# Optimization experiments

Hardware: AMD Instinct MI355X
Metric: run time of the kernel (lower is better)

## Reference

```python
import jax, jax.numpy as jnp
import numpy as np

SX = 4.0
SY = 4.0
H_DIM = 1024
B = 128
FH, FW = 24, 48


def setup_inputs() -> dict:
    key = jax.random.key(0)
    ks = jax.random.split(key, 8)
    s = lambda fan_in: 1.0 / np.sqrt(fan_in)
    return {
        "inp": jax.random.normal(ks[0], (B, H_DIM), jnp.float32),
        "hid": jax.random.normal(ks[1], (B, H_DIM), jnp.float32),
        "V": jax.random.normal(ks[2], (FH, FW, B, H_DIM), jnp.float32),
        "W1": jax.random.normal(ks[3], (2 * H_DIM, H_DIM), jnp.float32) * s(H_DIM),
        "b1": jnp.zeros((2 * H_DIM,), jnp.float32),
        "W2": jax.random.normal(ks[4], (2, 2 * H_DIM), jnp.float32) * s(2 * H_DIM),
        "b2": jnp.zeros((2,), jnp.float32),
        "Wc": jax.random.normal(ks[5], (H_DIM, 2 * H_DIM), jnp.float32) * s(2 * H_DIM),
        "bc": jnp.zeros((H_DIM,), jnp.float32),
    }


def reference(inp, hid, V, W1, b1, W2, b2, Wc, bc):
    h, w = V.shape[0], V.shape[1]
    # alignment MLP: Linear -> tanh -> Linear -> sigmoid, output [B, 2]
    algn = jax.nn.sigmoid(jnp.tanh(hid @ W1.T + b1) @ W2.T + b2)
    px, py = algn[:, 0], algn[:, 1]           # [B]
    x0 = (px * w)[:, None, None]              # [B,1,1]
    y0 = (py * h)[:, None, None]
    xs = jnp.arange(w, dtype=V.dtype)[None, None, :]   # [1,1,w]
    ys = jnp.arange(h, dtype=V.dtype)[None, :, None]   # [1,h,1]
    # Gaussian window weights over the feature map, [B,h,w]
    alpha = jnp.exp(-((xs - x0) ** 2 / (2.0 * SX * SX)
                      + (ys - y0) ** 2 / (2.0 * SY * SY)))
    alpha = alpha / alpha.sum(axis=(1, 2), keepdims=True)
    # weighted pooling over spatial dims: [B,h,w] x [h,w,B,H] -> [B,H]
    attn = jnp.einsum('brc,rcbh->bh', alpha, V)
    # contextualizer: Linear(2H, H) + ReLU on concat([inp, attn])
    ctx = jax.nn.relu(jnp.concatenate([inp, attn], axis=1) @ Wc.T + bc)
    return ctx
```

## Files before the change

### kernel.cpp

```cpp
#include <hip/hip_runtime.h>
#include <math.h>

#define NB 128
#define HD 1024
#define FHH 24
#define FWW 48

#define OFF_TPART 0u
#define OFF_X0    2097152u
#define OFF_Y0    2097280u
#define OFF_WXN   2097408u
#define OFF_WYN   2103552u
#define OFF_ATTN  2106624u

__global__ __launch_bounds__(256) void k_gemm1(
    const float* __restrict__ hid, const float* __restrict__ W1,
    float* __restrict__ tpart) {
  __shared__ float xs[32][132];
  __shared__ float wsh[32][36];
  const int tid = threadIdx.x;
  const int jt = blockIdx.x;
  const int ks = blockIdx.y;
  const int ty = tid >> 3, tx = tid & 7;
  const int b0 = ty * 4, jl = tx * 4;
  float acc[4][4] = {{0.f, 0.f, 0.f, 0.f}};
  for (int kt = 0; kt < 4; ++kt) {
    const int k0 = ks * 128 + kt * 32;
#pragma unroll
    for (int i = 0; i < 4; ++i) {
      int idx = tid + 256 * i;
      int bb = idx >> 3, q = idx & 7;
      float4 g = *(const float4*)(hid + bb * 1024 + k0 + q * 4);
      xs[q * 4 + 0][bb] = g.x;
      xs[q * 4 + 1][bb] = g.y;
      xs[q * 4 + 2][bb] = g.z;
      xs[q * 4 + 3][bb] = g.w;
    }
    {
      int o = tid >> 3, q = tid & 7;
      float4 g = *(const float4*)(W1 + (size_t)(jt * 32 + o) * 1024 + k0 + q * 4);
      wsh[q * 4 + 0][o] = g.x;
      wsh[q * 4 + 1][o] = g.y;
      wsh[q * 4 + 2][o] = g.z;
      wsh[q * 4 + 3][o] = g.w;
    }
    __syncthreads();
#pragma unroll
    for (int kk = 0; kk < 32; ++kk) {
      float4 xa = *(const float4*)&xs[kk][b0];
      float4 wb = *(const float4*)&wsh[kk][jl];
      acc[0][0] = fmaf(xa.x, wb.x, acc[0][0]);
      acc[0][1] = fmaf(xa.x, wb.y, acc[0][1]);
      acc[0][2] = fmaf(xa.x, wb.z, acc[0][2]);
      acc[0][3] = fmaf(xa.x, wb.w, acc[0][3]);
      acc[1][0] = fmaf(xa.y, wb.x, acc[1][0]);
      acc[1][1] = fmaf(xa.y, wb.y, acc[1][1]);
      acc[1][2] = fmaf(xa.y, wb.z, acc[1][2]);
      acc[1][3] = fmaf(xa.y, wb.w, acc[1][3]);
      acc[2][0] = fmaf(xa.z, wb.x, acc[2][0]);
      acc[2][1] = fmaf(xa.z, wb.y, acc[2][1]);
      acc[2][2] = fmaf(xa.z, wb.z, acc[2][2]);
      acc[2][3] = fmaf(xa.z, wb.w, acc[2][3]);
      acc[3][0] = fmaf(xa.w, wb.x, acc[3][0]);
      acc[3][1] = fmaf(xa.w, wb.y, acc[3][1]);
      acc[3][2] = fmaf(xa.w, wb.z, acc[3][2]);
      acc[3][3] = fmaf(xa.w, wb.w, acc[3][3]);
    }
    __syncthreads();
  }
#pragma unroll
  for (int u = 0; u < 4; ++u) {
    float4 o;
    o.x = acc[u][0]; o.y = acc[u][1]; o.z = acc[u][2]; o.w = acc[u][3];
    *(float4*)(tpart + (size_t)ks * 262144u + (size_t)(b0 + u) * 2048u +
               (jt * 32 + jl)) = o;
  }
}

__global__ __launch_bounds__(256) void k_align(
    const float* __restrict__ tpart, const float* __restrict__ b1,
    const float* __restrict__ W2, const float* __restrict__ b2,
    float* __restrict__ x0a, float* __restrict__ y0a,
    float* __restrict__ wxn, float* __restrict__ wyn) {
  const int b = blockIdx.x;
  const int tid = threadIdx.x;
  float a0 = 0.f, a1 = 0.f;
#pragma unroll
  for (int i = 0; i < 8; ++i) {
    int j = tid + 256 * i;
    float s = b1[j];
#pragma unroll
    for (int ks = 0; ks < 8; ++ks)
      s += tpart[(size_t)ks * 262144u + (size_t)b * 2048u + j];
    float tv = tanhf(s);
    a0 += tv * W2[j];
    a1 += tv * W2[2048 + j];
  }
  __shared__ float r0[256], r1[256];
  r0[tid] = a0; r1[tid] = a1;
  __syncthreads();
  for (int s = 128; s > 0; s >>= 1) {
    if (tid < s) { r0[tid] += r0[tid + s]; r1[tid] += r1[tid + s]; }
    __syncthreads();
  }
  __shared__ float xy[2];
  __shared__ float wxl[48], wyl[24];
  __shared__ float invZ[2];
  if (tid == 0) {
    float p0 = 1.f / (1.f + expf(-(r0[0] + b2[0])));
    float p1 = 1.f / (1.f + expf(-(r1[0] + b2[1])));
    xy[0] = p0 * 48.f;
    xy[1] = p1 * 24.f;
  }
  __syncthreads();
  float x0 = xy[0], y0 = xy[1];
  if (tid < 48) {
    float d = (float)tid - x0;
    wxl[tid] = expf(-d * d * (1.f / 32.f));
  } else if (tid >= 64 && tid < 88) {
    int r = tid - 64;
    float d = (float)r - y0;
    wyl[r] = expf(-d * d * (1.f / 32.f));
  }
  __syncthreads();
  if (tid == 0) {
    float zx = 0.f, zy = 0.f;
    for (int c = 0; c < 48; ++c) zx += wxl[c];
    for (int r = 0; r < 24; ++r) zy += wyl[r];
    invZ[0] = 1.f / zx;
    invZ[1] = 1.f / zy;
  }
  __syncthreads();
  if (tid < 48) wxn[b * 48 + tid] = wxl[tid] * invZ[0];
  else if (tid >= 64 && tid < 88) wyn[b * 24 + (tid - 64)] = wyl[tid - 64] * invZ[1];
  if (tid == 0) { x0a[b] = x0; y0a[b] = y0; }
}

__global__ __launch_bounds__(512) void k_attn(
    const float* __restrict__ V, const float* __restrict__ x0a,
    const float* __restrict__ y0a, const float* __restrict__ wxn,
    const float* __restrict__ wyn, float* __restrict__ attn) {
  const int b = blockIdx.x;
  const int qtr = blockIdx.y;
  const int tid = threadIdx.x;
  const int w = tid >> 6;
  const int lane = tid & 63;
  __shared__ float wxl[48], wyl[24];
  __shared__ float xy[2];
  __shared__ float red[8][260];
  if (tid < 48) wxl[tid] = wxn[b * 48 + tid];
  else if (tid >= 64 && tid < 88) wyl[tid - 64] = wyn[b * 24 + (tid - 64)];
  if (tid == 96) xy[0] = x0a[b];
  if (tid == 97) xy[1] = y0a[b];
  __syncthreads();
  const float x0 = xy[0], y0 = xy[1];
  const int h0 = qtr * 256 + lane * 4;
  float4 acc; acc.x = 0.f; acc.y = 0.f; acc.z = 0.f; acc.w = 0.f;
  const int rlo = max(0, (int)ceilf(y0 - 12.f));
  const int rhi = min(23, (int)floorf(y0 + 12.f));
  for (int r = w; r < 24; r += 8) {
    if (r < rlo || r > rhi) continue;
    float dy = (float)r - y0;
    float rad = sqrtf(fmaxf(144.f - dy * dy, 0.f));
    int c0 = max(0, (int)ceilf(x0 - rad));
    int c1 = min(47, (int)floorf(x0 + rad));
    float wy = wyl[r];
    const float* base = V + ((size_t)((r * 48 + c0) * 128 + b)) * 1024u + h0;
#pragma unroll 4
    for (int c = c0; c <= c1; ++c) {
      float wgt = wy * wxl[c];
      const float4 v = *(const float4*)(base + (size_t)(c - c0) * 131072u);
      acc.x = fmaf(wgt, v.x, acc.x);
      acc.y = fmaf(wgt, v.y, acc.y);
      acc.z = fmaf(wgt, v.z, acc.z);
      acc.w = fmaf(wgt, v.w, acc.w);
    }
  }
  *(float4*)&red[w][lane * 4] = acc;
  __syncthreads();
  if (tid < 256) {
    float s = 0.f;
#pragma unroll
    for (int ww = 0; ww < 8; ++ww) s += red[ww][tid];
    attn[(size_t)b * 1024u + qtr * 256 + tid] = s;
  }
}

__global__ __launch_bounds__(256) void k_gemm2(
    const float* __restrict__ inp, const float* __restrict__ attn,
    const float* __restrict__ Wc, float* __restrict__ psum) {
  __shared__ float xs[32][132];
  __shared__ float wsh[32][36];
  const int tid = threadIdx.x;
  const int ot = blockIdx.x;
  const int ks = blockIdx.y;
  const int ty = tid >> 3, tx = tid & 7;
  const int b0 = ty * 4, ol = tx * 4;
  const float* xsrc = (ks < 4) ? inp : attn;
  const int kbase = (ks < 4) ? ks * 256 : (ks - 4) * 256;
  float acc[4][4] = {{0.f, 0.f, 0.f, 0.f}};
  for (int kt = 0; kt < 8; ++kt) {
    const int k0g = ks * 256 + kt * 32;
    const int k0x = kbase + kt * 32;
#pragma unroll
    for (int i = 0; i < 4; ++i) {
      int idx = tid + 256 * i;
      int bb = idx >> 3, q = idx & 7;
      float4 g = *(const float4*)(xsrc + bb * 1024 + k0x + q * 4);
      xs[q * 4 + 0][bb] = g.x;
      xs[q * 4 + 1][bb] = g.y;
      xs[q * 4 + 2][bb] = g.z;
      xs[q * 4 + 3][bb] = g.w;
    }
    {
      int o = tid >> 3, q = tid & 7;
      float4 g = *(const float4*)(Wc + (size_t)(ot * 32 + o) * 2048u + k0g + q * 4);
      wsh[q * 4 + 0][o] = g.x;
      wsh[q * 4 + 1][o] = g.y;
      wsh[q * 4 + 2][o] = g.z;
      wsh[q * 4 + 3][o] = g.w;
    }
    __syncthreads();
#pragma unroll
    for (int kk = 0; kk < 32; ++kk) {
      float4 xa = *(const float4*)&xs[kk][b0];
      float4 wb = *(const float4*)&wsh[kk][ol];
      acc[0][0] = fmaf(xa.x, wb.x, acc[0][0]);
      acc[0][1] = fmaf(xa.x, wb.y, acc[0][1]);
      acc[0][2] = fmaf(xa.x, wb.z, acc[0][2]);
      acc[0][3] = fmaf(xa.x, wb.w, acc[0][3]);
      acc[1][0] = fmaf(xa.y, wb.x, acc[1][0]);
      acc[1][1] = fmaf(xa.y, wb.y, acc[1][1]);
      acc[1][2] = fmaf(xa.y, wb.z, acc[1][2]);
      acc[1][3] = fmaf(xa.y, wb.w, acc[1][3]);
      acc[2][0] = fmaf(xa.z, wb.x, acc[2][0]);
      acc[2][1] = fmaf(xa.z, wb.y, acc[2][1]);
      acc[2][2] = fmaf(xa.z, wb.z, acc[2][2]);
      acc[2][3] = fmaf(xa.z, wb.w, acc[2][3]);
      acc[3][0] = fmaf(xa.w, wb.x, acc[3][0]);
      acc[3][1] = fmaf(xa.w, wb.y, acc[3][1]);
      acc[3][2] = fmaf(xa.w, wb.z, acc[3][2]);
      acc[3][3] = fmaf(xa.w, wb.w, acc[3][3]);
    }
    __syncthreads();
  }
#pragma unroll
  for (int u = 0; u < 4; ++u) {
    float4 o;
    o.x = acc[u][0]; o.y = acc[u][1]; o.z = acc[u][2]; o.w = acc[u][3];
    *(float4*)(psum + (size_t)ks * 131072u + (size_t)(b0 + u) * 1024u +
               (ot * 32 + ol)) = o;
  }
}

__global__ __launch_bounds__(256) void k_final(
    const float* __restrict__ psum, const float* __restrict__ bc,
    float* __restrict__ out) {
  const int gid = blockIdx.x * 256 + threadIdx.x;
  const int o = gid & 1023;
  float s = bc[o];
#pragma unroll
  for (int i = 0; i < 8; ++i) s += psum[(size_t)i * 131072u + gid];
  out[gid] = fmaxf(s, 0.f);
}

extern "C" void kernel_launch(void* const* d_in, const int* in_sizes, int n_in,
                              void* d_out, int out_size, void* d_ws,
                              size_t ws_size, hipStream_t stream) {
  const float* inp = (const float*)d_in[0];
  const float* hid = (const float*)d_in[1];
  const float* V   = (const float*)d_in[2];
  const float* W1  = (const float*)d_in[3];
  const float* b1  = (const float*)d_in[4];
  const float* W2  = (const float*)d_in[5];
  const float* b2  = (const float*)d_in[6];
  const float* Wc  = (const float*)d_in[7];
  const float* bc  = (const float*)d_in[8];
  float* out = (float*)d_out;
  float* ws = (float*)d_ws;

  float* tpart = ws + OFF_TPART;
  float* x0a   = ws + OFF_X0;
  float* y0a   = ws + OFF_Y0;
  float* wxn   = ws + OFF_WXN;
  float* wyn   = ws + OFF_WYN;
  float* attn  = ws + OFF_ATTN;

  k_gemm1<<<dim3(64, 8), 256, 0, stream>>>(hid, W1, tpart);
  k_align<<<128, 256, 0, stream>>>(tpart, b1, W2, b2, x0a, y0a, wxn, wyn);
  k_attn<<<dim3(128, 4), 512, 0, stream>>>(V, x0a, y0a, wxn, wyn, attn);
  k_gemm2<<<dim3(32, 8), 256, 0, stream>>>(inp, attn, Wc, tpart);
  k_final<<<512, 256, 0, stream>>>(tpart, bc, out);
}
```

Baseline: 743.1 us.

## Flatten Gaussian window cells into balanced per-batch list for attention gather

k_align now computes the truncated window's cells once per batch: flat V offsets plus combined normalized weights, padded to a multiple of 64. k_attn stages this list in shared memory, and each warp walks an even, strided share of it with 8-way unrolled vector loads. This replaces the per-row split, where each warp took whole rows of uneven length and redid the bounds maths. Loads of V are marked nontemporal. The cost is extra workspace writes and reads for the cell list and a small amount of padded zero-weight work.

```diff
diff --git a/kernel.cpp b/kernel.cpp
--- a/kernel.cpp
+++ b/kernel.cpp
@@ -5,13 +5,15 @@
 #define HD 1024
 #define FHH 24
 #define FWW 48
+#define MAXCELL 640
+
+typedef float f4 __attribute__((ext_vector_type(4)));
 
 #define OFF_TPART 0u
-#define OFF_X0    2097152u
-#define OFF_Y0    2097280u
-#define OFF_WXN   2097408u
-#define OFF_WYN   2103552u
-#define OFF_ATTN  2106624u
+#define OFF_NC    2097152u
+#define OFF_COFF  2097280u
+#define OFF_CWTS  2179200u
+#define OFF_ATTN  2261120u
 
 __global__ __launch_bounds__(256) void k_gemm1(
     const float* __restrict__ hid, const float* __restrict__ W1,
@@ -80,8 +82,8 @@
 __global__ __launch_bounds__(256) void k_align(
     const float* __restrict__ tpart, const float* __restrict__ b1,
     const float* __restrict__ W2, const float* __restrict__ b2,
-    float* __restrict__ x0a, float* __restrict__ y0a,
-    float* __restrict__ wxn, float* __restrict__ wyn) {
+    int* __restrict__ ncnt, unsigned* __restrict__ goffs,
+    float* __restrict__ gwts) {
   const int b = blockIdx.x;
   const int tid = threadIdx.x;
   float a0 = 0.f, a1 = 0.f;
@@ -113,7 +115,7 @@
     xy[1] = p1 * 24.f;
   }
   __syncthreads();
-  float x0 = xy[0], y0 = xy[1];
+  const float x0 = xy[0], y0 = xy[1];
   if (tid < 48) {
     float d = (float)tid - x0;
     wxl[tid] = expf(-d * d * (1.f / 32.f));
@@ -131,52 +133,80 @@
     invZ[1] = 1.f / zy;
   }
   __syncthreads();
-  if (tid < 48) wxn[b * 48 + tid] = wxl[tid] * invZ[0];
-  else if (tid >= 64 && tid < 88) wyn[b * 24 + (tid - 64)] = wyl[tid - 64] * invZ[1];
-  if (tid == 0) { x0a[b] = x0; y0a[b] = y0; }
+  __shared__ int c0s[24], cnts[24], rowst[24];
+  __shared__ int tot[2];
+  const int rlo = max(0, (int)ceilf(y0 - 12.f));
+  const int rhi = min(23, (int)floorf(y0 + 12.f));
+  if (tid < 24) {
+    int cnt = 0, c0 = 0;
+    if (tid >= rlo && tid <= rhi) {
+      float dy = (float)tid - y0;
+      float rad = sqrtf(fmaxf(144.f - dy * dy, 0.f));
+      c0 = max(0, (int)ceilf(x0 - rad));
+      int c1 = min(47, (int)floorf(x0 + rad));
+      cnt = (c1 >= c0) ? (c1 - c0 + 1) : 0;
+    }
+    c0s[tid] = c0;
+    cnts[tid] = cnt;
+  }
+  __syncthreads();
+  if (tid == 0) {
+    int run = 0;
+    for (int r = 0; r < 24; ++r) { rowst[r] = run; run += cnts[r]; }
+    tot[0] = run;
+    tot[1] = (run + 63) & ~63;
+  }
+  __syncthreads();
+  const float izx = invZ[0], izy = invZ[1];
+#pragma unroll
+  for (int r = 0; r < 24; ++r) {
+    if (tid < cnts[r]) {
+      int c = c0s[r] + tid;
+      int e = rowst[r] + tid;
+      goffs[b * MAXCELL + e] = (unsigned)((r * 48 + c) * 128 + b) * 1024u;
+      gwts[b * MAXCELL + e] = (wyl[r] * izy) * (wxl[c] * izx);
+    }
+  }
+  for (int e = tot[0] + tid; e < tot[1]; e += 256) {
+    goffs[b * MAXCELL + e] = 0u;
+    gwts[b * MAXCELL + e] = 0.f;
+  }
+  if (tid == 0) ncnt[b] = tot[1];
 }
 
 __global__ __launch_bounds__(512) void k_attn(
-    const float* __restrict__ V, const float* __restrict__ x0a,
-    const float* __restrict__ y0a, const float* __restrict__ wxn,
-    const float* __restrict__ wyn, float* __restrict__ attn) {
+    const float* __restrict__ V, const int* __restrict__ ncnt,
+    const unsigned* __restrict__ goffs, const float* __restrict__ gwts,
+    float* __restrict__ attn) {
   const int b = blockIdx.x;
   const int qtr = blockIdx.y;
   const int tid = threadIdx.x;
   const int w = tid >> 6;
   const int lane = tid & 63;
-  __shared__ float wxl[48], wyl[24];
-  __shared__ float xy[2];
-  __shared__ float red[8][260];
-  if (tid < 48) wxl[tid] = wxn[b * 48 + tid];
-  else if (tid >= 64 && tid < 88) wyl[tid - 64] = wyn[b * 24 + (tid - 64)];
-  if (tid == 96) xy[0] = x0a[b];
-  if (tid == 97) xy[1] = y0a[b];
-  __syncthreads();
-  const float x0 = xy[0], y0 = xy[1];
+  __shared__ unsigned offs_l[MAXCELL];
+  __shared__ float wts_l[MAXCELL];
+  const int npad = ncnt[b];
+  for (int i = tid; i < npad; i += 512) {
+    offs_l[i] = goffs[b * MAXCELL + i];
+    wts_l[i] = gwts[b * MAXCELL + i];
+  }
+  __syncthreads();
   const int h0 = qtr * 256 + lane * 4;
-  float4 acc; acc.x = 0.f; acc.y = 0.f; acc.z = 0.f; acc.w = 0.f;
-  const int rlo = max(0, (int)ceilf(y0 - 12.f));
-  const int rhi = min(23, (int)floorf(y0 + 12.f));
-  for (int r = w; r < 24; r += 8) {
-    if (r < rlo || r > rhi) continue;
-    float dy = (float)r - y0;
-    float rad = sqrtf(fmaxf(144.f - dy * dy, 0.f));
-    int c0 = max(0, (int)ceilf(x0 - rad));
-    int c1 = min(47, (int)floorf(x0 + rad));
-    float wy = wyl[r];
-    const float* base = V + ((size_t)((r * 48 + c0) * 128 + b)) * 1024u + h0;
-#pragma unroll 4
-    for (int c = c0; c <= c1; ++c) {
-      float wgt = wy * wxl[c];
-      const float4 v = *(const float4*)(base + (size_t)(c - c0) * 131072u);
+  f4 acc = {0.f, 0.f, 0.f, 0.f};
+  for (int t = w * 8; t < npad; t += 64) {
+#pragma unroll
+    for (int u = 0; u < 8; ++u) {
+      unsigned off = offs_l[t + u];
+      float wgt = wts_l[t + u];
+      f4 v = __builtin_nontemporal_load((const f4*)(V + off + h0));
       acc.x = fmaf(wgt, v.x, acc.x);
       acc.y = fmaf(wgt, v.y, acc.y);
       acc.z = fmaf(wgt, v.z, acc.z);
       acc.w = fmaf(wgt, v.w, acc.w);
     }
   }
-  *(float4*)&red[w][lane * 4] = acc;
+  __shared__ float red[8][260];
+  *(f4*)&red[w][lane * 4] = acc;
   __syncthreads();
   if (tid < 256) {
     float s = 0.f;
@@ -279,16 +309,15 @@
   float* out = (float*)d_out;
   float* ws = (float*)d_ws;
 
-  float* tpart = ws + OFF_TPART;
-  float* x0a   = ws + OFF_X0;
-  float* y0a   = ws + OFF_Y0;
-  float* wxn   = ws + OFF_WXN;
-  float* wyn   = ws + OFF_WYN;
-  float* attn  = ws + OFF_ATTN;
+  float* tpart    = ws + OFF_TPART;
+  int* ncnt       = (int*)(ws + OFF_NC);
+  unsigned* goffs = (unsigned*)(ws + OFF_COFF);
+  float* gwts     = ws + OFF_CWTS;
+  float* attn     = ws + OFF_ATTN;
 
   k_gemm1<<<dim3(64, 8), 256, 0, stream>>>(hid, W1, tpart);
-  k_align<<<128, 256, 0, stream>>>(tpart, b1, W2, b2, x0a, y0a, wxn, wyn);
-  k_attn<<<dim3(128, 4), 512, 0, stream>>>(V, x0a, y0a, wxn, wyn, attn);
+  k_align<<<128, 256, 0, stream>>>(tpart, b1, W2, b2, ncnt, goffs, gwts);
+  k_attn<<<dim3(128, 4), 512, 0, stream>>>(V, ncnt, goffs, gwts, attn);
   k_gemm2<<<dim3(32, 8), 256, 0, stream>>>(inp, attn, Wc, tpart);
   k_final<<<512, 256, 0, stream>>>(tpart, bc, out);
 }
```

New measurement: 737.0 us. No clear change (-0.8%).
